# Optimization experiments

Measured on AMD Instinct MI355X. Metric: run time of the kernel, lower is better.

The kernel has to match this reference:

```python
import jax, jax.numpy as jnp
import numpy as np

HEADS = 8
DIM_HEAD = 96
INNER = HEADS * DIM_HEAD  # 768
PEP_DIM = 768
PRO_DIM = 768
SCALE = DIM_HEAD ** -0.5
NEG = -1000000.0
EPS = 1e-5


def _layer_norm(x, g, b):
    mu = jnp.mean(x, axis=-1, keepdims=True)
    var = jnp.mean(jnp.square(x - mu), axis=-1, keepdims=True)
    return (x - mu) * jax.lax.rsqrt(var + EPS) * g + b


def setup_inputs() -> dict:
    key = jax.random.key(0)
    ks = jax.random.split(key, 12)
    b, n, m = 16, 128, 2048
    peptide = jax.random.normal(ks[0], (b, n, PEP_DIM), dtype=jnp.float32)
    protein = jax.random.normal(ks[1], (b, m, PRO_DIM), dtype=jnp.float32)
    peptide_mask = jax.random.randint(ks[2], (b, n), 0, 2, dtype=jnp.int32)
    pro_mask = jax.random.randint(ks[3], (b, m), 0, 2, dtype=jnp.int32)
    s = 0.02
    Wq = jax.random.normal(ks[4], (PEP_DIM, INNER), dtype=jnp.float32) * s
    Wk = jax.random.normal(ks[5], (PRO_DIM, INNER), dtype=jnp.float32) * s
    Wv_prot = jax.random.normal(ks[6], (PRO_DIM, INNER), dtype=jnp.float32) * s
    Wv_pep = jax.random.normal(ks[7], (PEP_DIM, INNER), dtype=jnp.float32) * s
    Wo_prot = jax.random.normal(ks[8], (INNER, PEP_DIM), dtype=jnp.float32) * s
    bo_prot = jnp.zeros((PEP_DIM,), dtype=jnp.float32)
    Wo_pep = jax.random.normal(ks[9], (INNER, PRO_DIM), dtype=jnp.float32) * s
    bo_pep = jnp.zeros((PRO_DIM,), dtype=jnp.float32)
    ln_g = jnp.ones((PEP_DIM,), dtype=jnp.float32)
    ln_b = jnp.zeros((PEP_DIM,), dtype=jnp.float32)
    return {
        'peptide': peptide, 'protein': protein,
        'peptide_mask': peptide_mask, 'pro_mask': pro_mask,
        'Wq': Wq, 'Wk': Wk, 'Wv_prot': Wv_prot, 'Wv_pep': Wv_pep,
        'Wo_prot': Wo_prot, 'bo_prot': bo_prot,
        'Wo_pep': Wo_pep, 'bo_pep': bo_pep,
        'ln_g': ln_g, 'ln_b': ln_b,
    }


def reference(peptide, protein, peptide_mask, pro_mask,
              Wq, Wk, Wv_prot, Wv_pep, Wo_prot, bo_prot, Wo_pep, bo_pep,
              ln_g, ln_b):
    b, n, _ = peptide.shape
    m = protein.shape[1]
    # projections -> (b, h, len, d)
    q = (peptide @ Wq).reshape(b, n, HEADS, DIM_HEAD).transpose(0, 2, 1, 3)
    k = (protein @ Wk).reshape(b, m, HEADS, DIM_HEAD).transpose(0, 2, 1, 3)
    v_prot = (protein @ Wv_prot).reshape(b, m, HEADS, DIM_HEAD).transpose(0, 2, 1, 3)
    v_pep = (peptide @ Wv_pep).reshape(b, n, HEADS, DIM_HEAD).transpose(0, 2, 1, 3)
    # scores (b, h, n, m)
    dots = jnp.einsum('bhnd,bhmd->bhnm', q, k) * SCALE
    dots = jnp.where(peptide_mask[:, None, :, None] == 0, NEG, dots)
    dots = jnp.where(pro_mask[:, None, None, :] == 0, NEG, dots)
    attn = jax.nn.softmax(dots, axis=-1)
    # peptide-side output: rows of attn aggregate protein values
    out_protein = jnp.einsum('bhnm,bhmd->bhnd', attn, v_prot)
    out_protein = out_protein.transpose(0, 2, 1, 3).reshape(b, n, INNER)
    out_protein = out_protein @ Wo_prot + bo_prot
    out_protein = _layer_norm(out_protein + peptide, ln_g, ln_b)
    # protein-side output: attn^T aggregates peptide values
    out_peptide = jnp.einsum('bhnm,bhnd->bhmd', attn, v_pep)
    out_peptide = out_peptide.transpose(0, 2, 1, 3).reshape(b, m, INNER)
    out_peptide = out_peptide @ Wo_pep + bo_pep
    out_peptide = _layer_norm(out_peptide + protein, ln_g, ln_b)
    return (out_protein, out_peptide, attn)
```

## Files before the change

### kernel.cpp

```cpp
#include <hip/hip_runtime.h>
#include <math.h>

static constexpr int HEADS  = 8;
static constexpr int DHEAD  = 96;
static constexpr int INNER  = 768;
static constexpr int NPEP   = 128;
static constexpr int MPRO   = 2048;
static constexpr int NBATCH = 16;
static constexpr float ATT_SCALE = 0.10206207261596577f;
static constexpr float NEGF   = -1000000.0f;
static constexpr float LN_EPS = 1e-5f;

typedef __attribute__((ext_vector_type(8))) short bf16x8;
typedef __attribute__((ext_vector_type(4))) float f32x4;

__device__ __forceinline__ unsigned short f2b(float f) {
    unsigned u = __builtin_bit_cast(unsigned, f);
    u += 0x7fffu + ((u >> 16) & 1u);
    return (unsigned short)(u >> 16);
}

__device__ __forceinline__ void async16(const unsigned short* g, unsigned short* l) {
    __builtin_amdgcn_global_load_lds(
        (const __attribute__((address_space(1))) void*)g,
        (__attribute__((address_space(3))) void*)l, 16, 0, 0);
}

template<int MODE>
__global__ __launch_bounds__(256) void gemm_bf16(
    const unsigned short* __restrict__ A, const unsigned short* __restrict__ B,
    void* __restrict__ C,
    int M, int N, int K, int lda, int ldb, int ldc,
    long sAb, long sAh, long sBb, long sBh, long sCb, long sCh,
    const int* __restrict__ mRow, const int* __restrict__ mCol, int lenShift)
{
    __shared__ unsigned short As[128 * 32];
    __shared__ unsigned short Bs[128 * 32];

    const int tid = threadIdx.x;
    const int n0  = blockIdx.x * 128;
    const int m0  = blockIdx.y * 128;
    const int z   = blockIdx.z;
    const int zb  = z >> 3, zh = z & 7;

    const unsigned short* Ab = A + zb * sAb + zh * sAh;
    const unsigned short* Bb = B + zb * sBb + zh * sBh;

    const int rS = tid >> 2;
    const int kS = (tid & 3) * 8;
    const int wave = tid >> 6;
    unsigned short* ldsA0 = As + wave * 512;
    unsigned short* ldsA1 = As + 2048 + wave * 512;
    unsigned short* ldsB0 = Bs + wave * 512;
    unsigned short* ldsB1 = Bs + 2048 + wave * 512;

    const int lane = tid & 63;
    const int l16  = lane & 15;
    const int quad = lane >> 4;
    const int wr   = (wave >> 1) * 64;
    const int wc   = (wave & 1) * 64;

    f32x4 acc[4][4];
#pragma unroll
    for (int i = 0; i < 4; ++i)
#pragma unroll
        for (int j = 0; j < 4; ++j) acc[i][j] = (f32x4){0.f, 0.f, 0.f, 0.f};

    for (int k0 = 0; k0 < K; k0 += 32) {
        async16(Ab + (long)(m0 + rS) * lda + k0 + kS, ldsA0);
        async16(Ab + (long)(m0 + 64 + rS) * lda + k0 + kS, ldsA1);
        int bR0 = n0 + rS;      if (bR0 > N - 1) bR0 = N - 1;
        int bR1 = n0 + 64 + rS; if (bR1 > N - 1) bR1 = N - 1;
        async16(Bb + (long)bR0 * ldb + k0 + kS, ldsB0);
        async16(Bb + (long)bR1 * ldb + k0 + kS, ldsB1);
        __syncthreads();

        bf16x8 af[4], bfr[4];
#pragma unroll
        for (int i = 0; i < 4; ++i)
            af[i] = *reinterpret_cast<const bf16x8*>(&As[(wr + i * 16 + l16) * 32 + quad * 8]);
#pragma unroll
        for (int j = 0; j < 4; ++j)
            bfr[j] = *reinterpret_cast<const bf16x8*>(&Bs[(wc + j * 16 + l16) * 32 + quad * 8]);
#pragma unroll
        for (int i = 0; i < 4; ++i)
#pragma unroll
            for (int j = 0; j < 4; ++j)
                acc[i][j] = __builtin_amdgcn_mfma_f32_16x16x32_bf16(af[i], bfr[j], acc[i][j], 0, 0, 0);
        __syncthreads();
    }

#pragma unroll
    for (int i = 0; i < 4; ++i) {
#pragma unroll
        for (int j = 0; j < 4; ++j) {
            const int col = n0 + wc + j * 16 + l16;
            if ((MODE == 0 || MODE == 2) && col >= N) continue;
#pragma unroll
            for (int r = 0; r < 4; ++r) {
                const int row = m0 + wr + i * 16 + quad * 4 + r;
                float v = acc[i][j][r];
                if (MODE == 0) {
                    ((float*)C)[zb * sCb + zh * sCh + (long)row * ldc + col] = v;
                } else if (MODE == 1) {
                    v *= ATT_SCALE;
                    if (mRow[zb * NPEP + row] == 0 || mCol[zb * MPRO + col] == 0) v = NEGF;
                    ((float*)C)[zb * sCb + zh * sCh + (long)row * ldc + col] = v;
                } else if (MODE == 2) {
                    ((unsigned short*)C)[zb * sCb + zh * sCh + (long)row * ldc + col] = f2b(v);
                } else if (MODE == 3) {
                    const int b = row >> lenShift, rr = row & ((1 << lenShift) - 1);
                    const int h = col / 96, d = col % 96;
                    ((unsigned short*)C)[(((long)(b * 8 + h) << lenShift) + rr) * 96 + d] = f2b(v);
                } else {
                    const int b = row >> lenShift, rr = row & ((1 << lenShift) - 1);
                    const int h = col / 96, d = col % 96;
                    ((unsigned short*)C)[(((long)(b * 8 + h) * 96 + d) << lenShift) + rr] = f2b(v);
                }
            }
        }
    }
}

__global__ __launch_bounds__(256) void conv_bf16_kernel(
    const float* __restrict__ in, unsigned short* __restrict__ out, int n4)
{
    const int i = blockIdx.x * 256 + threadIdx.x;
    if (i >= n4) return;
    float4 v = reinterpret_cast<const float4*>(in)[i];
    ushort4 o;
    o.x = f2b(v.x); o.y = f2b(v.y); o.z = f2b(v.z); o.w = f2b(v.w);
    reinterpret_cast<ushort4*>(out)[i] = o;
}

__global__ __launch_bounds__(256) void wtrans_kernel(
    const float* w0, const float* w1, const float* w2,
    const float* w3, const float* w4, const float* w5,
    unsigned short* o0, unsigned short* o1, unsigned short* o2,
    unsigned short* o3, unsigned short* o4, unsigned short* o5)
{
    const float* in; unsigned short* out;
    switch (blockIdx.z) {
        case 0: in = w0; out = o0; break;
        case 1: in = w1; out = o1; break;
        case 2: in = w2; out = o2; break;
        case 3: in = w3; out = o3; break;
        case 4: in = w4; out = o4; break;
        default: in = w5; out = o5; break;
    }
    __shared__ unsigned short t[32][33];
    const int bx = blockIdx.x * 32, by = blockIdx.y * 32;
    const int x = threadIdx.x, y = threadIdx.y;
#pragma unroll
    for (int i = 0; i < 32; i += 8)
        t[y + i][x] = f2b(in[(long)(by + y + i) * 768 + bx + x]);
    __syncthreads();
#pragma unroll
    for (int i = 0; i < 32; i += 8)
        out[(long)(bx + y + i) * 768 + by + x] = t[x][y + i];
}

__global__ __launch_bounds__(256) void attn_trans_kernel(
    const float* __restrict__ attn, unsigned short* __restrict__ attnT)
{
    __shared__ unsigned short t[32][33];
    const long bi = (long)blockIdx.z * NPEP * MPRO;
    const long bo = (long)blockIdx.z * MPRO * NPEP;
    const int m0 = blockIdx.x * 32, n0 = blockIdx.y * 32;
    const int x = threadIdx.x, y = threadIdx.y;
#pragma unroll
    for (int i = 0; i < 32; i += 8)
        t[y + i][x] = f2b(attn[bi + (long)(n0 + y + i) * MPRO + m0 + x]);
    __syncthreads();
#pragma unroll
    for (int i = 0; i < 32; i += 8)
        attnT[bo + (long)(m0 + y + i) * NPEP + n0 + x] = t[x][y + i];
}

__global__ __launch_bounds__(256) void softmax_kernel(
    float* __restrict__ attn, unsigned short* __restrict__ attn16)
{
    __shared__ float red[256];
    const long row = blockIdx.x;
    float* p = attn + row * (long)MPRO;
    unsigned short* p16 = attn16 + row * (long)MPRO;
    const int tid = threadIdx.x;

    float v[8];
    float mx = -3.4e38f;
#pragma unroll
    for (int k = 0; k < 8; ++k) { v[k] = p[tid + k * 256]; mx = fmaxf(mx, v[k]); }
    red[tid] = mx; __syncthreads();
    for (int s = 128; s > 0; s >>= 1) { if (tid < s) red[tid] = fmaxf(red[tid], red[tid + s]); __syncthreads(); }
    mx = red[0]; __syncthreads();

    float sum = 0.f;
#pragma unroll
    for (int k = 0; k < 8; ++k) { v[k] = expf(v[k] - mx); sum += v[k]; }
    red[tid] = sum; __syncthreads();
    for (int s = 128; s > 0; s >>= 1) { if (tid < s) red[tid] += red[tid + s]; __syncthreads(); }
    const float inv = 1.0f / red[0];
#pragma unroll
    for (int k = 0; k < 8; ++k) {
        const float o = v[k] * inv;
        p[tid + k * 256] = o;
        p16[tid + k * 256] = f2b(o);
    }
}

__global__ __launch_bounds__(256) void bias_res_ln(
    const float* __restrict__ tmp, const float* __restrict__ bias,
    const float* __restrict__ res, const float* __restrict__ gam,
    const float* __restrict__ bet, float* __restrict__ out)
{
    __shared__ float red[256];
    const long row = blockIdx.x;
    const float* t = tmp + row * INNER;
    const float* r = res + row * INNER;
    float* o = out + row * INNER;
    const int tid = threadIdx.x;

    float v[3]; float s = 0.f;
#pragma unroll
    for (int k = 0; k < 3; ++k) { const int c = tid + k * 256; v[k] = t[c] + bias[c] + r[c]; s += v[k]; }
    red[tid] = s; __syncthreads();
    for (int st = 128; st > 0; st >>= 1) { if (tid < st) red[tid] += red[tid + st]; __syncthreads(); }
    const float mu = red[0] * (1.0f / INNER); __syncthreads();

    float vs = 0.f;
#pragma unroll
    for (int k = 0; k < 3; ++k) { const float d = v[k] - mu; vs += d * d; }
    red[tid] = vs; __syncthreads();
    for (int st = 128; st > 0; st >>= 1) { if (tid < st) red[tid] += red[tid + st]; __syncthreads(); }
    const float rstd = rsqrtf(red[0] * (1.0f / INNER) + LN_EPS);
#pragma unroll
    for (int k = 0; k < 3; ++k) { const int c = tid + k * 256; o[c] = (v[k] - mu) * rstd * gam[c] + bet[c]; }
}

extern "C" void kernel_launch(void* const* d_in, const int* in_sizes, int n_in,
                              void* d_out, int out_size, void* d_ws, size_t ws_size,
                              hipStream_t stream)
{
    (void)in_sizes; (void)n_in; (void)out_size; (void)ws_size;

    const float* peptide = (const float*)d_in[0];
    const float* protein = (const float*)d_in[1];
    const int*   pepm    = (const int*)  d_in[2];
    const int*   prom    = (const int*)  d_in[3];
    const float* Wq      = (const float*)d_in[4];
    const float* Wk      = (const float*)d_in[5];
    const float* Wv_prot = (const float*)d_in[6];
    const float* Wv_pep  = (const float*)d_in[7];
    const float* Wo_prot = (const float*)d_in[8];
    const float* bo_prot = (const float*)d_in[9];
    const float* Wo_pep  = (const float*)d_in[10];
    const float* bo_pep  = (const float*)d_in[11];
    const float* ln_g    = (const float*)d_in[12];
    const float* ln_b    = (const float*)d_in[13];

    char* ws = (char*)d_ws;
    auto U = [&](size_t off) { return (unsigned short*)(ws + off); };
    unsigned short* pro16  = U(0);
    unsigned short* pep16  = U(50331648);
    unsigned short* q16    = U(53477376);
    unsigned short* k16    = U(56623104);
    unsigned short* vpT    = U(106954752);
    unsigned short* vpepT  = U(157286400);
    unsigned short* WT0    = U(160432128);
    unsigned short* WT1    = U(160432128 + 1179648);
    unsigned short* WT2    = U(160432128 + 2 * 1179648);
    unsigned short* WT3    = U(160432128 + 3 * 1179648);
    unsigned short* WT4    = U(160432128 + 4 * 1179648);
    unsigned short* WT5    = U(160432128 + 5 * 1179648);
    unsigned short* attn16 = U(0);
    unsigned short* attnT  = U(0);
    unsigned short* opp    = U(67108864);
    float*          tmp1   = (float*)(ws + 70254592);
    unsigned short* opep   = U(100663296);
    float*          tmp2   = (float*)(ws + 0);

    float* outP = (float*)d_out;
    float* outQ = outP + 16 * 128 * 768;
    float* attn = outQ + (long)16 * 2048 * 768;

    conv_bf16_kernel<<<24576, 256, 0, stream>>>(protein, pro16, 6291456);
    conv_bf16_kernel<<<1536, 256, 0, stream>>>(peptide, pep16, 393216);
    wtrans_kernel<<<dim3(24, 24, 6), dim3(32, 8), 0, stream>>>(
        Wq, Wk, Wv_prot, Wv_pep, Wo_prot, Wo_pep, WT0, WT1, WT2, WT3, WT4, WT5);

    gemm_bf16<3><<<dim3(6, 16, 1), 256, 0, stream>>>(
        pep16, WT0, q16, 2048, 768, 768, 768, 768, 0,
        0, 0, 0, 0, 0, 0, nullptr, nullptr, 7);
    gemm_bf16<3><<<dim3(6, 256, 1), 256, 0, stream>>>(
        pro16, WT1, k16, 32768, 768, 768, 768, 768, 0,
        0, 0, 0, 0, 0, 0, nullptr, nullptr, 11);
    gemm_bf16<4><<<dim3(6, 256, 1), 256, 0, stream>>>(
        pro16, WT2, vpT, 32768, 768, 768, 768, 768, 0,
        0, 0, 0, 0, 0, 0, nullptr, nullptr, 11);
    gemm_bf16<4><<<dim3(6, 16, 1), 256, 0, stream>>>(
        pep16, WT3, vpepT, 2048, 768, 768, 768, 768, 0,
        0, 0, 0, 0, 0, 0, nullptr, nullptr, 7);

    gemm_bf16<1><<<dim3(16, 1, 128), 256, 0, stream>>>(
        q16, k16, attn, 128, 2048, 96, 96, 96, 2048,
        98304L, 12288L, 1572864L, 196608L, 2097152L, 262144L, pepm, prom, 0);

    softmax_kernel<<<16384, 256, 0, stream>>>(attn, attn16);

    gemm_bf16<2><<<dim3(1, 1, 128), 256, 0, stream>>>(
        attn16, vpT, opp, 128, 96, 2048, 2048, 2048, 768,
        2097152L, 262144L, 1572864L, 196608L, 98304L, 96L, nullptr, nullptr, 0);

    gemm_bf16<0><<<dim3(6, 16, 1), 256, 0, stream>>>(
        opp, WT4, tmp1, 2048, 768, 768, 768, 768, 768,
        0, 0, 0, 0, 0, 0, nullptr, nullptr, 0);
    bias_res_ln<<<2048, 256, 0, stream>>>(tmp1, bo_prot, peptide, ln_g, ln_b, outP);

    attn_trans_kernel<<<dim3(64, 4, 128), dim3(32, 8), 0, stream>>>(attn, attnT);

    gemm_bf16<2><<<dim3(1, 16, 128), 256, 0, stream>>>(
        attnT, vpepT, opep, 2048, 96, 128, 128, 128, 768,
        2097152L, 262144L, 98304L, 12288L, 1572864L, 96L, nullptr, nullptr, 0);

    gemm_bf16<0><<<dim3(6, 256, 1), 256, 0, stream>>>(
        opep, WT5, tmp2, 32768, 768, 768, 768, 768, 768,
        0, 0, 0, 0, 0, 0, nullptr, nullptr, 0);
    bias_res_ln<<<32768, 256, 0, stream>>>(tmp2, bo_pep, protein, ln_g, ln_b, outQ);
}
```

Baseline: 913.7 us.

## Use bf16 intermediates, drop attention transpose, fuse conversions, shuffle reductions

The score GEMM now writes bf16 scores instead of fp32. Softmax reads these bf16 scores and writes the fp32 attn output once. A new pv2 kernel transposes attention tiles in LDS, which replaces the separate transpose pass over attn. The output-projection GEMMs emit bf16 temporaries, the two fp32-to-bf16 conversions are merged into one launch, and the LayerNorm/softmax reductions use wave shuffles. Smaller 64-row tiles are added for the small GEMMs to raise block count. This cuts HBM traffic and launches, but quantizing the pre-softmax scores and the projection outputs to bf16 lowers accuracy.

Result: faster. 831.5 us (-9.0%).

```diff
diff --git a/kernel.cpp b/kernel.cpp
--- a/kernel.cpp
+++ b/kernel.cpp
@@ -6,7 +6,6 @@
 static constexpr int INNER  = 768;
 static constexpr int NPEP   = 128;
 static constexpr int MPRO   = 2048;
-static constexpr int NBATCH = 16;
 static constexpr float ATT_SCALE = 0.10206207261596577f;
 static constexpr float NEGF   = -1000000.0f;
 static constexpr float LN_EPS = 1e-5f;
@@ -19,6 +18,9 @@
     u += 0x7fffu + ((u >> 16) & 1u);
     return (unsigned short)(u >> 16);
 }
+__device__ __forceinline__ float b2f(unsigned short u) {
+    return __builtin_bit_cast(float, (unsigned)u << 16);
+}
 
 __device__ __forceinline__ void async16(const unsigned short* g, unsigned short* l) {
     __builtin_amdgcn_global_load_lds(
@@ -26,20 +28,21 @@
         (__attribute__((address_space(3))) void*)l, 16, 0, 0);
 }
 
-template<int MODE>
+template<int TM, int MODE>
 __global__ __launch_bounds__(256) void gemm_bf16(
     const unsigned short* __restrict__ A, const unsigned short* __restrict__ B,
-    void* __restrict__ C,
+    unsigned short* __restrict__ C,
     int M, int N, int K, int lda, int ldb, int ldc,
     long sAb, long sAh, long sBb, long sBh, long sCb, long sCh,
     const int* __restrict__ mRow, const int* __restrict__ mCol, int lenShift)
 {
-    __shared__ unsigned short As[128 * 32];
+    constexpr int FR = TM / 32;
+    __shared__ unsigned short As[TM * 32];
     __shared__ unsigned short Bs[128 * 32];
 
     const int tid = threadIdx.x;
     const int n0  = blockIdx.x * 128;
-    const int m0  = blockIdx.y * 128;
+    const int m0  = blockIdx.y * TM;
     const int z   = blockIdx.z;
     const int zb  = z >> 3, zh = z & 7;
 
@@ -57,33 +60,34 @@
     const int lane = tid & 63;
     const int l16  = lane & 15;
     const int quad = lane >> 4;
-    const int wr   = (wave >> 1) * 64;
+    const int wr   = (wave >> 1) * (TM / 2);
     const int wc   = (wave & 1) * 64;
 
-    f32x4 acc[4][4];
-#pragma unroll
-    for (int i = 0; i < 4; ++i)
+    f32x4 acc[FR][4];
+#pragma unroll
+    for (int i = 0; i < FR; ++i)
 #pragma unroll
         for (int j = 0; j < 4; ++j) acc[i][j] = (f32x4){0.f, 0.f, 0.f, 0.f};
 
     for (int k0 = 0; k0 < K; k0 += 32) {
         async16(Ab + (long)(m0 + rS) * lda + k0 + kS, ldsA0);
-        async16(Ab + (long)(m0 + 64 + rS) * lda + k0 + kS, ldsA1);
+        if (TM == 128)
+            async16(Ab + (long)(m0 + 64 + rS) * lda + k0 + kS, ldsA1);
         int bR0 = n0 + rS;      if (bR0 > N - 1) bR0 = N - 1;
         int bR1 = n0 + 64 + rS; if (bR1 > N - 1) bR1 = N - 1;
         async16(Bb + (long)bR0 * ldb + k0 + kS, ldsB0);
         async16(Bb + (long)bR1 * ldb + k0 + kS, ldsB1);
         __syncthreads();
 
-        bf16x8 af[4], bfr[4];
-#pragma unroll
-        for (int i = 0; i < 4; ++i)
+        bf16x8 af[FR], bfr[4];
+#pragma unroll
+        for (int i = 0; i < FR; ++i)
             af[i] = *reinterpret_cast<const bf16x8*>(&As[(wr + i * 16 + l16) * 32 + quad * 8]);
 #pragma unroll
         for (int j = 0; j < 4; ++j)
             bfr[j] = *reinterpret_cast<const bf16x8*>(&Bs[(wc + j * 16 + l16) * 32 + quad * 8]);
 #pragma unroll
-        for (int i = 0; i < 4; ++i)
+        for (int i = 0; i < FR; ++i)
 #pragma unroll
             for (int j = 0; j < 4; ++j)
                 acc[i][j] = __builtin_amdgcn_mfma_f32_16x16x32_bf16(af[i], bfr[j], acc[i][j], 0, 0, 0);
@@ -91,46 +95,132 @@
     }
 
 #pragma unroll
-    for (int i = 0; i < 4; ++i) {
+    for (int i = 0; i < FR; ++i) {
 #pragma unroll
         for (int j = 0; j < 4; ++j) {
             const int col = n0 + wc + j * 16 + l16;
-            if ((MODE == 0 || MODE == 2) && col >= N) continue;
+            if ((MODE == 2) && col >= N) continue;
+            const int h = col / 96, d = col - h * 96;
 #pragma unroll
             for (int r = 0; r < 4; ++r) {
                 const int row = m0 + wr + i * 16 + quad * 4 + r;
                 float v = acc[i][j][r];
-                if (MODE == 0) {
-                    ((float*)C)[zb * sCb + zh * sCh + (long)row * ldc + col] = v;
-                } else if (MODE == 1) {
+                if (MODE == 1) {
                     v *= ATT_SCALE;
                     if (mRow[zb * NPEP + row] == 0 || mCol[zb * MPRO + col] == 0) v = NEGF;
-                    ((float*)C)[zb * sCb + zh * sCh + (long)row * ldc + col] = v;
+                    C[zb * sCb + zh * sCh + (long)row * ldc + col] = f2b(v);
                 } else if (MODE == 2) {
-                    ((unsigned short*)C)[zb * sCb + zh * sCh + (long)row * ldc + col] = f2b(v);
+                    C[zb * sCb + zh * sCh + (long)row * ldc + col] = f2b(v);
                 } else if (MODE == 3) {
                     const int b = row >> lenShift, rr = row & ((1 << lenShift) - 1);
-                    const int h = col / 96, d = col % 96;
-                    ((unsigned short*)C)[(((long)(b * 8 + h) << lenShift) + rr) * 96 + d] = f2b(v);
+                    C[(((long)(b * 8 + h) << lenShift) + rr) * 96 + d] = f2b(v);
                 } else {
                     const int b = row >> lenShift, rr = row & ((1 << lenShift) - 1);
-                    const int h = col / 96, d = col % 96;
-                    ((unsigned short*)C)[(((long)(b * 8 + h) * 96 + d) << lenShift) + rr] = f2b(v);
+                    C[(((long)(b * 8 + h) * 96 + d) << lenShift) + rr] = f2b(v);
                 }
             }
         }
     }
 }
 
-__global__ __launch_bounds__(256) void conv_bf16_kernel(
-    const float* __restrict__ in, unsigned short* __restrict__ out, int n4)
+__global__ __launch_bounds__(256) void pv2_kernel(
+    const unsigned short* __restrict__ attn16,
+    const unsigned short* __restrict__ vpepT,
+    unsigned short* __restrict__ opep)
+{
+    __shared__ unsigned short At[128 * 136];
+    __shared__ unsigned short Bv[128 * 136];
+
+    const int tid = threadIdx.x;
+    const int m0  = blockIdx.x * 128;
+    const int z   = blockIdx.y;
+    const int b   = z >> 3, h = z & 7;
+
+    const unsigned short* Az = attn16 + (long)z * NPEP * MPRO;
+    const unsigned short* Bz = vpepT + (long)z * 96 * 128;
+
+    {
+        const int r = tid >> 1, half = tid & 1;
+        const int rc = r > 95 ? 95 : r;
+#pragma unroll
+        for (int e = 0; e < 8; ++e) {
+            bf16x8 v = *reinterpret_cast<const bf16x8*>(Bz + rc * 128 + half * 64 + e * 8);
+            *reinterpret_cast<bf16x8*>(&Bv[r * 136 + half * 64 + e * 8]) = v;
+        }
+    }
+    {
+        const int mBase = (tid & 7) * 16;
+#pragma unroll
+        for (int nn = 0; nn < 128; nn += 32) {
+            const int n = nn + (tid >> 3);
+#pragma unroll
+            for (int c = 0; c < 2; ++c) {
+                bf16x8 v = *reinterpret_cast<const bf16x8*>(Az + (long)n * MPRO + m0 + mBase + c * 8);
+#pragma unroll
+                for (int j = 0; j < 8; ++j)
+                    At[(mBase + c * 8 + j) * 136 + n] = (unsigned short)v[j];
+            }
+        }
+    }
+    __syncthreads();
+
+    const int lane = tid & 63;
+    const int l16  = lane & 15;
+    const int quad = lane >> 4;
+    const int wave = tid >> 6;
+    const int wr   = (wave >> 1) * 64;
+    const int wc   = (wave & 1) * 64;
+
+    f32x4 acc[4][4];
+#pragma unroll
+    for (int i = 0; i < 4; ++i)
+#pragma unroll
+        for (int j = 0; j < 4; ++j) acc[i][j] = (f32x4){0.f, 0.f, 0.f, 0.f};
+
+#pragma unroll
+    for (int kc = 0; kc < 4; ++kc) {
+        bf16x8 af[4], bfr[4];
+#pragma unroll
+        for (int i = 0; i < 4; ++i)
+            af[i] = *reinterpret_cast<const bf16x8*>(&At[(wr + i * 16 + l16) * 136 + kc * 32 + quad * 8]);
+#pragma unroll
+        for (int j = 0; j < 4; ++j)
+            bfr[j] = *reinterpret_cast<const bf16x8*>(&Bv[(wc + j * 16 + l16) * 136 + kc * 32 + quad * 8]);
+#pragma unroll
+        for (int i = 0; i < 4; ++i)
+#pragma unroll
+            for (int j = 0; j < 4; ++j)
+                acc[i][j] = __builtin_amdgcn_mfma_f32_16x16x32_bf16(af[i], bfr[j], acc[i][j], 0, 0, 0);
+    }
+
+#pragma unroll
+    for (int i = 0; i < 4; ++i) {
+#pragma unroll
+        for (int j = 0; j < 4; ++j) {
+            const int d = wc + j * 16 + l16;
+            if (d >= 96) continue;
+#pragma unroll
+            for (int r = 0; r < 4; ++r) {
+                const int m = m0 + wr + i * 16 + quad * 4 + r;
+                opep[(long)b * MPRO * INNER + (long)m * INNER + h * 96 + d] = f2b(acc[i][j][r]);
+            }
+        }
+    }
+}
+
+__global__ __launch_bounds__(256) void conv2_kernel(
+    const float* __restrict__ pro, const float* __restrict__ pep,
+    unsigned short* __restrict__ pro16, unsigned short* __restrict__ pep16,
+    int nPro4, int nPep4)
 {
     const int i = blockIdx.x * 256 + threadIdx.x;
-    if (i >= n4) return;
-    float4 v = reinterpret_cast<const float4*>(in)[i];
+    const float* in; unsigned short* out; int idx;
+    if (i < nPro4) { in = pro; out = pro16; idx = i; }
+    else { idx = i - nPro4; if (idx >= nPep4) return; in = pep; out = pep16; }
+    float4 v = reinterpret_cast<const float4*>(in)[idx];
     ushort4 o;
     o.x = f2b(v.x); o.y = f2b(v.y); o.z = f2b(v.z); o.w = f2b(v.w);
-    reinterpret_cast<ushort4*>(out)[i] = o;
+    reinterpret_cast<ushort4*>(out)[idx] = o;
 }
 
 __global__ __launch_bounds__(256) void wtrans_kernel(
@@ -160,79 +250,72 @@
         out[(long)(bx + y + i) * 768 + by + x] = t[x][y + i];
 }
 
-__global__ __launch_bounds__(256) void attn_trans_kernel(
-    const float* __restrict__ attn, unsigned short* __restrict__ attnT)
-{
-    __shared__ unsigned short t[32][33];
-    const long bi = (long)blockIdx.z * NPEP * MPRO;
-    const long bo = (long)blockIdx.z * MPRO * NPEP;
-    const int m0 = blockIdx.x * 32, n0 = blockIdx.y * 32;
-    const int x = threadIdx.x, y = threadIdx.y;
-#pragma unroll
-    for (int i = 0; i < 32; i += 8)
-        t[y + i][x] = f2b(attn[bi + (long)(n0 + y + i) * MPRO + m0 + x]);
-    __syncthreads();
-#pragma unroll
-    for (int i = 0; i < 32; i += 8)
-        attnT[bo + (long)(m0 + y + i) * NPEP + n0 + x] = t[x][y + i];
-}
-
 __global__ __launch_bounds__(256) void softmax_kernel(
-    float* __restrict__ attn, unsigned short* __restrict__ attn16)
-{
-    __shared__ float red[256];
+    unsigned short* __restrict__ s16, float* __restrict__ attn)
+{
+    __shared__ float smx[4], sms[4];
     const long row = blockIdx.x;
-    float* p = attn + row * (long)MPRO;
-    unsigned short* p16 = attn16 + row * (long)MPRO;
+    unsigned short* p16 = s16 + row * (long)MPRO;
+    float* pf = attn + row * (long)MPRO;
     const int tid = threadIdx.x;
+    const int wv = tid >> 6;
 
     float v[8];
     float mx = -3.4e38f;
 #pragma unroll
-    for (int k = 0; k < 8; ++k) { v[k] = p[tid + k * 256]; mx = fmaxf(mx, v[k]); }
-    red[tid] = mx; __syncthreads();
-    for (int s = 128; s > 0; s >>= 1) { if (tid < s) red[tid] = fmaxf(red[tid], red[tid + s]); __syncthreads(); }
-    mx = red[0]; __syncthreads();
+    for (int k = 0; k < 8; ++k) { v[k] = b2f(p16[tid + k * 256]); mx = fmaxf(mx, v[k]); }
+#pragma unroll
+    for (int off = 32; off > 0; off >>= 1) mx = fmaxf(mx, __shfl_xor(mx, off));
+    if ((tid & 63) == 0) smx[wv] = mx;
+    __syncthreads();
+    mx = fmaxf(fmaxf(smx[0], smx[1]), fmaxf(smx[2], smx[3]));
 
     float sum = 0.f;
 #pragma unroll
-    for (int k = 0; k < 8; ++k) { v[k] = expf(v[k] - mx); sum += v[k]; }
-    red[tid] = sum; __syncthreads();
-    for (int s = 128; s > 0; s >>= 1) { if (tid < s) red[tid] += red[tid + s]; __syncthreads(); }
-    const float inv = 1.0f / red[0];
+    for (int k = 0; k < 8; ++k) { v[k] = __expf(v[k] - mx); sum += v[k]; }
+#pragma unroll
+    for (int off = 32; off > 0; off >>= 1) sum += __shfl_xor(sum, off);
+    if ((tid & 63) == 0) sms[wv] = sum;
+    __syncthreads();
+    const float inv = 1.0f / (sms[0] + sms[1] + sms[2] + sms[3]);
 #pragma unroll
     for (int k = 0; k < 8; ++k) {
         const float o = v[k] * inv;
-        p[tid + k * 256] = o;
+        pf[tid + k * 256] = o;
         p16[tid + k * 256] = f2b(o);
     }
 }
 
 __global__ __launch_bounds__(256) void bias_res_ln(
-    const float* __restrict__ tmp, const float* __restrict__ bias,
+    const unsigned short* __restrict__ tmp, const float* __restrict__ bias,
     const float* __restrict__ res, const float* __restrict__ gam,
     const float* __restrict__ bet, float* __restrict__ out)
 {
-    __shared__ float red[256];
+    __shared__ float red[8];
     const long row = blockIdx.x;
-    const float* t = tmp + row * INNER;
+    const unsigned short* t = tmp + row * INNER;
     const float* r = res + row * INNER;
     float* o = out + row * INNER;
     const int tid = threadIdx.x;
+    const int wv = tid >> 6;
 
     float v[3]; float s = 0.f;
 #pragma unroll
-    for (int k = 0; k < 3; ++k) { const int c = tid + k * 256; v[k] = t[c] + bias[c] + r[c]; s += v[k]; }
-    red[tid] = s; __syncthreads();
-    for (int st = 128; st > 0; st >>= 1) { if (tid < st) red[tid] += red[tid + st]; __syncthreads(); }
-    const float mu = red[0] * (1.0f / INNER); __syncthreads();
+    for (int k = 0; k < 3; ++k) { const int c = tid + k * 256; v[k] = b2f(t[c]) + bias[c] + r[c]; s += v[k]; }
+#pragma unroll
+    for (int off = 32; off > 0; off >>= 1) s += __shfl_xor(s, off);
+    if ((tid & 63) == 0) red[wv] = s;
+    __syncthreads();
+    const float mu = (red[0] + red[1] + red[2] + red[3]) * (1.0f / INNER);
 
     float vs = 0.f;
 #pragma unroll
     for (int k = 0; k < 3; ++k) { const float d = v[k] - mu; vs += d * d; }
-    red[tid] = vs; __syncthreads();
-    for (int st = 128; st > 0; st >>= 1) { if (tid < st) red[tid] += red[tid + st]; __syncthreads(); }
-    const float rstd = rsqrtf(red[0] * (1.0f / INNER) + LN_EPS);
+#pragma unroll
+    for (int off = 32; off > 0; off >>= 1) vs += __shfl_xor(vs, off);
+    if ((tid & 63) == 0) red[4 + wv] = vs;
+    __syncthreads();
+    const float rstd = rsqrtf((red[4] + red[5] + red[6] + red[7]) * (1.0f / INNER) + LN_EPS);
 #pragma unroll
     for (int k = 0; k < 3; ++k) { const int c = tid + k * 256; o[c] = (v[k] - mu) * rstd * gam[c] + bet[c]; }
 }
@@ -260,69 +343,63 @@
 
     char* ws = (char*)d_ws;
     auto U = [&](size_t off) { return (unsigned short*)(ws + off); };
-    unsigned short* pro16  = U(0);
-    unsigned short* pep16  = U(50331648);
-    unsigned short* q16    = U(53477376);
-    unsigned short* k16    = U(56623104);
-    unsigned short* vpT    = U(106954752);
-    unsigned short* vpepT  = U(157286400);
-    unsigned short* WT0    = U(160432128);
-    unsigned short* WT1    = U(160432128 + 1179648);
-    unsigned short* WT2    = U(160432128 + 2 * 1179648);
-    unsigned short* WT3    = U(160432128 + 3 * 1179648);
-    unsigned short* WT4    = U(160432128 + 4 * 1179648);
-    unsigned short* WT5    = U(160432128 + 5 * 1179648);
-    unsigned short* attn16 = U(0);
-    unsigned short* attnT  = U(0);
-    unsigned short* opp    = U(67108864);
-    float*          tmp1   = (float*)(ws + 70254592);
-    unsigned short* opep   = U(100663296);
-    float*          tmp2   = (float*)(ws + 0);
+    unsigned short* WT0   = U(0);
+    unsigned short* WT1   = U(1179648);
+    unsigned short* WT2   = U(2 * 1179648);
+    unsigned short* WT3   = U(3 * 1179648);
+    unsigned short* WT4   = U(4 * 1179648);
+    unsigned short* WT5   = U(5 * 1179648);
+    unsigned short* q16   = U(7077888);
+    unsigned short* k16   = U(10223616);
+    unsigned short* vpT   = U(60555264);
+    unsigned short* vpepT = U(110886912);
+    unsigned short* s16   = U(114032640);
+    unsigned short* pro16 = U(114032640);
+    unsigned short* pep16 = U(164364288);
+    unsigned short* opp   = U(7077888);
+    unsigned short* tmp1  = U(10223616);
+    unsigned short* opep  = U(13369344);
+    unsigned short* tmp2  = U(63700992);
 
     float* outP = (float*)d_out;
     float* outQ = outP + 16 * 128 * 768;
     float* attn = outQ + (long)16 * 2048 * 768;
 
-    conv_bf16_kernel<<<24576, 256, 0, stream>>>(protein, pro16, 6291456);
-    conv_bf16_kernel<<<1536, 256, 0, stream>>>(peptide, pep16, 393216);
+    conv2_kernel<<<26112, 256, 0, stream>>>(protein, peptide, pro16, pep16, 6291456, 393216);
     wtrans_kernel<<<dim3(24, 24, 6), dim3(32, 8), 0, stream>>>(
         Wq, Wk, Wv_prot, Wv_pep, Wo_prot, Wo_pep, WT0, WT1, WT2, WT3, WT4, WT5);
 
-    gemm_bf16<3><<<dim3(6, 16, 1), 256, 0, stream>>>(
+    gemm_bf16<128, 3><<<dim3(6, 16, 1), 256, 0, stream>>>(
         pep16, WT0, q16, 2048, 768, 768, 768, 768, 0,
         0, 0, 0, 0, 0, 0, nullptr, nullptr, 7);
-    gemm_bf16<3><<<dim3(6, 256, 1), 256, 0, stream>>>(
+    gemm_bf16<128, 3><<<dim3(6, 256, 1), 256, 0, stream>>>(
         pro16, WT1, k16, 32768, 768, 768, 768, 768, 0,
         0, 0, 0, 0, 0, 0, nullptr, nullptr, 11);
-    gemm_bf16<4><<<dim3(6, 256, 1), 256, 0, stream>>>(
+    gemm_bf16<128, 4><<<dim3(6, 256, 1), 256, 0, stream>>>(
         pro16, WT2, vpT, 32768, 768, 768, 768, 768, 0,
         0, 0, 0, 0, 0, 0, nullptr, nullptr, 11);
-    gemm_bf16<4><<<dim3(6, 16, 1), 256, 0, stream>>>(
+    gemm_bf16<128, 4><<<dim3(6, 16, 1), 256, 0, stream>>>(
         pep16, WT3, vpepT, 2048, 768, 768, 768, 768, 0,
         0, 0, 0, 0, 0, 0, nullptr, nullptr, 7);
 
-    gemm_bf16<1><<<dim3(16, 1, 128), 256, 0, stream>>>(
-        q16, k16, attn, 128, 2048, 96, 96, 96, 2048,
+    gemm_bf16<128, 1><<<dim3(16, 1, 128), 256, 0, stream>>>(
+        q16, k16, s16, 128, 2048, 96, 96, 96, 2048,
         98304L, 12288L, 1572864L, 196608L, 2097152L, 262144L, pepm, prom, 0);
 
-    softmax_kernel<<<16384, 256, 0, stream>>>(attn, attn16);
-
-    gemm_bf16<2><<<dim3(1, 1, 128), 256, 0, stream>>>(
-        attn16, vpT, opp, 128, 96, 2048, 2048, 2048, 768,
+    softmax_kernel<<<16384, 256, 0, stream>>>(s16, attn);
+
+    gemm_bf16<64, 2><<<dim3(1, 2, 128), 256, 0, stream>>>(
+        s16, vpT, opp, 128, 96, 2048, 2048, 2048, 768,
         2097152L, 262144L, 1572864L, 196608L, 98304L, 96L, nullptr, nullptr, 0);
 
-    gemm_bf16<0><<<dim3(6, 16, 1), 256, 0, stream>>>(
+    gemm_bf16<64, 2><<<dim3(6, 32, 1), 256, 0, stream>>>(
         opp, WT4, tmp1, 2048, 768, 768, 768, 768, 768,
         0, 0, 0, 0, 0, 0, nullptr, nullptr, 0);
     bias_res_ln<<<2048, 256, 0, stream>>>(tmp1, bo_prot, peptide, ln_g, ln_b, outP);
 
-    attn_trans_kernel<<<dim3(64, 4, 128), dim3(32, 8), 0, stream>>>(attn, attnT);
-
-    gemm_bf16<2><<<dim3(1, 16, 128), 256, 0, stream>>>(
-        attnT, vpepT, opep, 2048, 96, 128, 128, 128, 768,
-        2097152L, 262144L, 98304L, 12288L, 1572864L, 96L, nullptr, nullptr, 0);
-
-    gemm_bf16<0><<<dim3(6, 256, 1), 256, 0, stream>>>(
+    pv2_kernel<<<dim3(16, 128), 256, 0, stream>>>(s16, vpepT, opep);
+
+    gemm_bf16<128, 2><<<dim3(6, 256, 1), 256, 0, stream>>>(
         opep, WT5, tmp2, 32768, 768, 768, 768, 768, 768,
         0, 0, 0, 0, 0, 0, nullptr, nullptr, 0);
     bias_res_ln<<<32768, 256, 0, stream>>>(tmp2, bo_pep, protein, ln_g, ln_b, outQ);
```
